# Optimization experiments

Measured on AMD Instinct MI355X. Metric: run time of the kernel, lower is better.

The kernel has to match this reference:

```python
import jax, jax.numpy as jnp
import numpy as np

BN_EPS = 1e-5
LEAKY_SLOPE = 0.01

N_TOTAL, FEAT_DIM = 100000, 128
N_BATCH, K = 50000, 16
EMBED_DIM = 128


def setup_inputs() -> dict:
    key = jax.random.key(0)
    k1, k2, k3 = jax.random.split(key, 3)
    raw_features = jax.random.normal(k1, (N_TOTAL, FEAT_DIM), dtype=jnp.float32)
    weight = jax.random.normal(k2, (FEAT_DIM, EMBED_DIM), dtype=jnp.float32) * (1.0 / np.sqrt(FEAT_DIM))
    gamma = jnp.ones((EMBED_DIM,), dtype=jnp.float32)
    beta = jnp.zeros((EMBED_DIM,), dtype=jnp.float32)
    neigh_idx = jax.random.randint(k3, (N_BATCH, K), 0, N_TOTAL, dtype=jnp.int64)
    return {"raw_features": raw_features, "weight": weight, "gamma": gamma,
            "beta": beta, "neigh_idx": neigh_idx}


def reference(raw_features, weight, gamma, beta, neigh_idx):
    # Mean aggregation over sampled neighbors: [N_BATCH, K, F] -> [N_BATCH, F]
    neigh_feats = jnp.mean(raw_features[neigh_idx], axis=1)
    # Dense transform: [N_BATCH, EMBED_DIM]
    x = neigh_feats @ weight
    # BatchNorm1d (training mode: batch statistics, biased variance)
    mean = jnp.mean(x, axis=0)
    var = jnp.var(x, axis=0)
    x = (x - mean) * jax.lax.rsqrt(var + BN_EPS) * gamma + beta
    # LeakyReLU (default negative_slope=0.01)
    return jnp.where(x >= 0, x, LEAKY_SLOPE * x)
```

## Files before the change

### kernel.cpp

```cpp
#include <hip/hip_runtime.h>
#include <hip/hip_bf16.h>


#define NTOTAL 100000
#define FEAT   128
#define NB     50000
#define KNEI   16
#define NTILES (NB / 16)
#define ZTILES (NTOTAL / 16)
#define NSLOT  8

#define OFF_PSTAT 0
#define OFF_ZB    8192
#define OFF_XB    (8192 + 25600000)
#define WS_NEEDED (OFF_XB + 12800000)

typedef float f32x4 __attribute__((ext_vector_type(4)));
typedef short bf16x8 __attribute__((ext_vector_type(8)));

__device__ __forceinline__ unsigned short f2bf(float f) {
    union { float f; unsigned u; } v; v.f = f;
    unsigned r = v.u + 0x7FFF + ((v.u >> 16) & 1);
    return (unsigned short)(r >> 16);
}

#define WT_LD 136
#define A_LD  136

__global__ __launch_bounds__(256, 4) void enc_zgemm(
    const float* __restrict__ raw, const float* __restrict__ W,
    unsigned short* __restrict__ Zb, float* __restrict__ pstats)
{
    __shared__ unsigned short sWt[128 * WT_LD];
    __shared__ unsigned short sA[16 * A_LD];

    const int t = threadIdx.x;

    if (blockIdx.x == 0) {
        #pragma unroll
        for (int i = 0; i < NSLOT; ++i) pstats[t + i * 256] = 0.f;
    }

    #pragma unroll
    for (int i = 0; i < 16; ++i) {
        int e = t + i * 256;
        float4 w4 = ((const float4*)W)[e];
        int li = e * 4;
        int k = li >> 7, n = li & 127;
        sWt[(n + 0) * WT_LD + k] = f2bf(w4.x);
        sWt[(n + 1) * WT_LD + k] = f2bf(w4.y);
        sWt[(n + 2) * WT_LD + k] = f2bf(w4.z);
        sWt[(n + 3) * WT_LD + k] = f2bf(w4.w);
    }

    const int lane = t & 63;
    const int wv = t >> 6;
    const int ln = lane & 15;
    const int qd = lane >> 4;
    const int c2 = t & 15;
    const int g  = t >> 4;
    const int n0 = wv * 32 + ln, n1 = n0 + 16;

    for (int tile = blockIdx.x; tile < ZTILES; tile += gridDim.x) {
        const int r0 = tile * 16;
        __syncthreads();
        {
            const float4* rp = (const float4*)&raw[(size_t)(r0 + g) * FEAT + c2 * 8];
            float4 x0 = rp[0], x1 = rp[1];
            uint4 b;
            b.x = (unsigned)f2bf(x0.x) | ((unsigned)f2bf(x0.y) << 16);
            b.y = (unsigned)f2bf(x0.z) | ((unsigned)f2bf(x0.w) << 16);
            b.z = (unsigned)f2bf(x1.x) | ((unsigned)f2bf(x1.y) << 16);
            b.w = (unsigned)f2bf(x1.z) | ((unsigned)f2bf(x1.w) << 16);
            *(uint4*)&sA[g * A_LD + c2 * 8] = b;
        }
        __syncthreads();

        f32x4 acc0 = {0.f, 0.f, 0.f, 0.f}, acc1 = {0.f, 0.f, 0.f, 0.f};
        #pragma unroll
        for (int kt = 0; kt < 4; ++kt) {
            const int k0 = kt * 32 + qd * 8;
            bf16x8 a  = *(const bf16x8*)&sA[ln * A_LD + k0];
            bf16x8 b0 = *(const bf16x8*)&sWt[n0 * WT_LD + k0];
            bf16x8 b1 = *(const bf16x8*)&sWt[n1 * WT_LD + k0];
            acc0 = __builtin_amdgcn_mfma_f32_16x16x32_bf16(a, b0, acc0, 0, 0, 0);
            acc1 = __builtin_amdgcn_mfma_f32_16x16x32_bf16(a, b1, acc1, 0, 0, 0);
        }

        #pragma unroll
        for (int ri = 0; ri < 4; ++ri) {
            const int row = r0 + qd * 4 + ri;
            Zb[row * FEAT + n0] = f2bf(acc0[ri]);
            Zb[row * FEAT + n1] = f2bf(acc1[ri]);
        }
    }
}

__global__ __launch_bounds__(256, 4) void enc_gather(
    const unsigned short* __restrict__ Zb, const int* __restrict__ idx,
    unsigned short* __restrict__ xb, float* __restrict__ pstats)
{
    __shared__ int sidx[256];
    __shared__ float sRed[4 * 256];

    const int t = threadIdx.x;
    const int i0 = blockIdx.x * 16;

    sidx[t] = idx[i0 * KNEI + t];
    __syncthreads();

    const int g = t >> 4, c2 = t & 15;
    const int* ip = &sidx[g * KNEI];

    uint4 v[16];
    #pragma unroll
    for (int k = 0; k < KNEI; ++k)
        v[k] = *(const uint4*)&Zb[(size_t)ip[k] * FEAT + c2 * 8];
    __builtin_amdgcn_sched_group_barrier(0x20, 16, 0);
    __builtin_amdgcn_sched_barrier(0);

    float a[8];
    #pragma unroll
    for (int j = 0; j < 8; ++j) a[j] = 0.f;
    #pragma unroll
    for (int k = 0; k < KNEI; ++k) {
        a[0] += __uint_as_float(v[k].x << 16);
        a[1] += __uint_as_float(v[k].x & 0xFFFF0000u);
        a[2] += __uint_as_float(v[k].y << 16);
        a[3] += __uint_as_float(v[k].y & 0xFFFF0000u);
        a[4] += __uint_as_float(v[k].z << 16);
        a[5] += __uint_as_float(v[k].z & 0xFFFF0000u);
        a[6] += __uint_as_float(v[k].w << 16);
        a[7] += __uint_as_float(v[k].w & 0xFFFF0000u);
    }
    #pragma unroll
    for (int j = 0; j < 8; ++j) a[j] *= 0.0625f;

    {
        uint4 b;
        b.x = (unsigned)f2bf(a[0]) | ((unsigned)f2bf(a[1]) << 16);
        b.y = (unsigned)f2bf(a[2]) | ((unsigned)f2bf(a[3]) << 16);
        b.z = (unsigned)f2bf(a[4]) | ((unsigned)f2bf(a[5]) << 16);
        b.w = (unsigned)f2bf(a[6]) | ((unsigned)f2bf(a[7]) << 16);
        *(uint4*)&xb[(size_t)(i0 + g) * FEAT + c2 * 8] = b;
    }

    float q[8];
    #pragma unroll
    for (int j = 0; j < 8; ++j) q[j] = a[j] * a[j];
    #pragma unroll
    for (int j = 0; j < 8; ++j) {
        a[j] += __shfl_down(a[j], 32); a[j] += __shfl_down(a[j], 16);
        q[j] += __shfl_down(q[j], 32); q[j] += __shfl_down(q[j], 16);
    }
    const int lane = t & 63, wv = t >> 6;
    if (lane < 16) {
        #pragma unroll
        for (int j = 0; j < 8; ++j) {
            sRed[wv * 256 + c2 * 8 + j]       = a[j];
            sRed[wv * 256 + 128 + c2 * 8 + j] = q[j];
        }
    }
    __syncthreads();
    float s = sRed[t] + sRed[256 + t] + sRed[512 + t] + sRed[768 + t];
    atomicAdd(&pstats[(blockIdx.x & (NSLOT - 1)) * 256 + t], s);
}

__global__ __launch_bounds__(256) void enc_bn(
    const unsigned short* __restrict__ xb, float* __restrict__ out,
    const float* __restrict__ pstats,
    const float* __restrict__ gamma, const float* __restrict__ beta)
{
    __shared__ float sScale[FEAT], sShift[FEAT];
    const int t = threadIdx.x;
    if (t < FEAT) {
        float s1 = 0.f, s2 = 0.f;
        #pragma unroll
        for (int sl = 0; sl < NSLOT; ++sl) {
            s1 += pstats[sl * 256 + t];
            s2 += pstats[sl * 256 + 128 + t];
        }
        float mean = s1 * (1.0f / NB);
        float var = s2 * (1.0f / NB) - mean * mean;
        float sc = gamma[t] * rsqrtf(var + 1e-5f);
        sScale[t] = sc;
        sShift[t] = beta[t] - mean * sc;
    }
    __syncthreads();

    const int f8 = (t & 15) * 8;
    const float4 sc0 = *(const float4*)&sScale[f8], sc1 = *(const float4*)&sScale[f8 + 4];
    const float4 sh0 = *(const float4*)&sShift[f8], sh1 = *(const float4*)&sShift[f8 + 4];

    const uint4* x4 = (const uint4*)xb;
    float4* o4 = (float4*)out;
    const int total8 = NB * FEAT / 8;
    for (int e = blockIdx.x * 256 + t; e < total8; e += gridDim.x * 256) {
        uint4 v = x4[e];
        float4 r0, r1; float y;
        y = __uint_as_float(v.x << 16)        * sc0.x + sh0.x; r0.x = (y >= 0.f) ? y : 0.01f * y;
        y = __uint_as_float(v.x & 0xFFFF0000u)* sc0.y + sh0.y; r0.y = (y >= 0.f) ? y : 0.01f * y;
        y = __uint_as_float(v.y << 16)        * sc0.z + sh0.z; r0.z = (y >= 0.f) ? y : 0.01f * y;
        y = __uint_as_float(v.y & 0xFFFF0000u)* sc0.w + sh0.w; r0.w = (y >= 0.f) ? y : 0.01f * y;
        y = __uint_as_float(v.z << 16)        * sc1.x + sh1.x; r1.x = (y >= 0.f) ? y : 0.01f * y;
        y = __uint_as_float(v.z & 0xFFFF0000u)* sc1.y + sh1.y; r1.y = (y >= 0.f) ? y : 0.01f * y;
        y = __uint_as_float(v.w << 16)        * sc1.z + sh1.z; r1.z = (y >= 0.f) ? y : 0.01f * y;
        y = __uint_as_float(v.w & 0xFFFF0000u)* sc1.w + sh1.w; r1.w = (y >= 0.f) ? y : 0.01f * y;
        o4[e * 2] = r0; o4[e * 2 + 1] = r1;
    }
}

__global__ __launch_bounds__(256, 4) void enc_gemm_f(
    const float* __restrict__ raw, const float* __restrict__ W,
    const int* __restrict__ idx, float* __restrict__ out,
    float* __restrict__ gstats)
{
    __shared__ unsigned short sWt[128 * WT_LD];
    __shared__ unsigned short sA[16 * A_LD];
    __shared__ int sidx[256];
    const int t = threadIdx.x;
    #pragma unroll 4
    for (int i = 0; i < 64; ++i) {
        int e = t + i * 256;
        int f = e >> 7, n = e & 127;
        sWt[n * WT_LD + f] = f2bf(W[e]);
    }
    const int lane = t & 63, wv = t >> 6, ln = lane & 15, qd = lane >> 4;
    const int c = t & 31, g = t >> 5;
    const int n0 = wv * 32 + ln, n1 = n0 + 16;
    float s1a = 0.f, s2a = 0.f, s1b = 0.f, s2b = 0.f;
    const float4* raw4 = (const float4*)raw;
    for (int tile = blockIdx.x; tile < NTILES; tile += gridDim.x) {
        const int i0 = tile * 16;
        __syncthreads();
        sidx[t] = idx[i0 * KNEI + t];
        __syncthreads();
        #pragma unroll
        for (int rr = 0; rr < 2; ++rr) {
            const int r = g * 2 + rr;
            const int* ip = &sidx[r * KNEI];
            float4 acc = {0.f, 0.f, 0.f, 0.f};
            #pragma unroll
            for (int k = 0; k < KNEI; ++k) {
                float4 v = raw4[(size_t)ip[k] * 32 + c];
                acc.x += v.x; acc.y += v.y; acc.z += v.z; acc.w += v.w;
            }
            ushort4 b;
            b.x = f2bf(acc.x * 0.0625f); b.y = f2bf(acc.y * 0.0625f);
            b.z = f2bf(acc.z * 0.0625f); b.w = f2bf(acc.w * 0.0625f);
            *(ushort4*)&sA[r * A_LD + c * 4] = b;
        }
        __syncthreads();
        f32x4 acc0 = {0.f, 0.f, 0.f, 0.f}, acc1 = {0.f, 0.f, 0.f, 0.f};
        #pragma unroll
        for (int kt = 0; kt < 4; ++kt) {
            const int k0 = kt * 32 + qd * 8;
            bf16x8 a  = *(const bf16x8*)&sA[ln * A_LD + k0];
            bf16x8 b0 = *(const bf16x8*)&sWt[n0 * WT_LD + k0];
            bf16x8 b1 = *(const bf16x8*)&sWt[n1 * WT_LD + k0];
            acc0 = __builtin_amdgcn_mfma_f32_16x16x32_bf16(a, b0, acc0, 0, 0, 0);
            acc1 = __builtin_amdgcn_mfma_f32_16x16x32_bf16(a, b1, acc1, 0, 0, 0);
        }
        #pragma unroll
        for (int ri = 0; ri < 4; ++ri) {
            const int row = i0 + qd * 4 + ri;
            float v0 = acc0[ri], v1 = acc1[ri];
            out[row * FEAT + n0] = v0;
            out[row * FEAT + n1] = v1;
            s1a += v0; s2a += v0 * v0;
            s1b += v1; s2b += v1 * v1;
        }
    }
    s1a += __shfl_down(s1a, 32); s1a += __shfl_down(s1a, 16);
    s2a += __shfl_down(s2a, 32); s2a += __shfl_down(s2a, 16);
    s1b += __shfl_down(s1b, 32); s1b += __shfl_down(s1b, 16);
    s2b += __shfl_down(s2b, 32); s2b += __shfl_down(s2b, 16);
    if (qd == 0) {
        atomicAdd(&gstats[n0], s1a);
        atomicAdd(&gstats[FEAT + n0], s2a);
        atomicAdd(&gstats[n1], s1b);
        atomicAdd(&gstats[FEAT + n1], s2b);
    }
}

__global__ __launch_bounds__(256) void enc_bn_f(
    float* __restrict__ out, const float* __restrict__ gstats,
    const float* __restrict__ gamma, const float* __restrict__ beta)
{
    __shared__ float sScale[FEAT], sShift[FEAT];
    const int t = threadIdx.x;
    if (t < FEAT) {
        float s1 = gstats[t], s2 = gstats[FEAT + t];
        float mean = s1 * (1.0f / NB);
        float var = s2 * (1.0f / NB) - mean * mean;
        float sc = gamma[t] * rsqrtf(var + 1e-5f);
        sScale[t] = sc;
        sShift[t] = beta[t] - mean * sc;
    }
    __syncthreads();
    const int f4 = (t & 31) * 4;
    const float4 sc = *(const float4*)&sScale[f4];
    const float4 sh = *(const float4*)&sShift[f4];
    const int total4 = NB * FEAT / 4;
    float4* o4 = (float4*)out;
    for (int e = blockIdx.x * 256 + t; e < total4; e += gridDim.x * 256) {
        float4 v = o4[e];
        float4 r; float y;
        y = v.x * sc.x + sh.x; r.x = (y >= 0.f) ? y : 0.01f * y;
        y = v.y * sc.y + sh.y; r.y = (y >= 0.f) ? y : 0.01f * y;
        y = v.z * sc.z + sh.z; r.z = (y >= 0.f) ? y : 0.01f * y;
        y = v.w * sc.w + sh.w; r.w = (y >= 0.f) ? y : 0.01f * y;
        o4[e] = r;
    }
}

extern "C" void kernel_launch(void* const* d_in, const int* in_sizes, int n_in,
                              void* d_out, int out_size, void* d_ws, size_t ws_size,
                              hipStream_t stream) {
    const float* raw   = (const float*)d_in[0];
    const float* W     = (const float*)d_in[1];
    const float* gamma = (const float*)d_in[2];
    const float* beta  = (const float*)d_in[3];
    const int*   idx   = (const int*)d_in[4];
    float* out = (float*)d_out;

    char* ws = (char*)d_ws;

    if (ws_size >= WS_NEEDED) {
        float* pstats        = (float*)(ws + OFF_PSTAT);
        unsigned short* Zb   = (unsigned short*)(ws + OFF_ZB);
        unsigned short* xb   = (unsigned short*)(ws + OFF_XB);
        enc_zgemm<<<1042, 256, 0, stream>>>(raw, W, Zb, pstats);
        enc_gather<<<NTILES, 256, 0, stream>>>(Zb, idx, xb, pstats);
        enc_bn<<<1024, 256, 0, stream>>>(xb, out, pstats, gamma, beta);
    } else {
        float* gstats = (float*)(ws + OFF_PSTAT);
        hipMemsetAsync(gstats, 0, 2 * FEAT * sizeof(float), stream);
        enc_gemm_f<<<1024, 256, 0, stream>>>(raw, W, idx, out, gstats);
        enc_bn_f<<<1024, 256, 0, stream>>>(out, gstats, gamma, beta);
    }
}
```

Measured before the change: 152.3 us.

## Fuse GEMM, gather and batchnorm into one cooperative kernel with grid syncs

```diff
diff --git a/kernel.cpp b/kernel.cpp
--- a/kernel.cpp
+++ b/kernel.cpp
@@ -1,5 +1,8 @@
 #include <hip/hip_runtime.h>
 #include <hip/hip_bf16.h>
+#include <hip/hip_cooperative_groups.h>
+
+namespace cg = cooperative_groups;
 
 
 #define NTOTAL 100000
@@ -9,6 +12,7 @@
 #define NTILES (NB / 16)
 #define ZTILES (NTOTAL / 16)
 #define NSLOT  8
+#define TMAX   4
 
 #define OFF_PSTAT 0
 #define OFF_ZB    8192
@@ -26,14 +30,22 @@
 
 #define WT_LD 136
 #define A_LD  136
-
-__global__ __launch_bounds__(256, 4) void enc_zgemm(
+#define SMEM_BYTES 39168
+
+__global__ __launch_bounds__(256, 4) void enc_all(
     const float* __restrict__ raw, const float* __restrict__ W,
+    const float* __restrict__ gamma, const float* __restrict__ beta,
+    const int* __restrict__ idx, float* __restrict__ out,
     unsigned short* __restrict__ Zb, float* __restrict__ pstats)
 {
-    __shared__ unsigned short sWt[128 * WT_LD];
-    __shared__ unsigned short sA[16 * A_LD];
-
+    __shared__ __align__(16) char smem[SMEM_BYTES];
+    unsigned short* sWt = (unsigned short*)smem;
+    unsigned short* sA  = (unsigned short*)(smem + 34816);
+    int*   sidx = (int*)smem;
+    float* sRed = (float*)(smem + 1024);
+    float* sSS  = (float*)smem;
+
+    cg::grid_group grid = cg::this_grid();
     const int t = threadIdx.x;
 
     if (blockIdx.x == 0) {
@@ -94,6 +106,176 @@
             Zb[row * FEAT + n1] = f2bf(acc1[ri]);
         }
     }
+    grid.sync();
+
+    uint4 xr0 = {0,0,0,0}, xr1 = {0,0,0,0}, xr2 = {0,0,0,0}, xr3 = {0,0,0,0};
+    float s1[8], s2[8];
+    #pragma unroll
+    for (int j = 0; j < 8; ++j) { s1[j] = 0.f; s2[j] = 0.f; }
+
+    #pragma unroll
+    for (int tt = 0; tt < TMAX; ++tt) {
+        const int tile = blockIdx.x + tt * gridDim.x;
+        if (tile < NTILES) {
+            __syncthreads();
+            sidx[t] = idx[tile * 16 * KNEI + t];
+            __syncthreads();
+
+            const int* ip = &sidx[g * KNEI];
+            uint4 v[16];
+            #pragma unroll
+            for (int k = 0; k < KNEI; ++k)
+                v[k] = *(const uint4*)&Zb[(size_t)ip[k] * FEAT + c2 * 8];
+            __builtin_amdgcn_sched_barrier(0);
+
+            float a[8];
+            #pragma unroll
+            for (int j = 0; j < 8; ++j) a[j] = 0.f;
+            #pragma unroll
+            for (int k = 0; k < KNEI; ++k) {
+                a[0] += __uint_as_float(v[k].x << 16);
+                a[1] += __uint_as_float(v[k].x & 0xFFFF0000u);
+                a[2] += __uint_as_float(v[k].y << 16);
+                a[3] += __uint_as_float(v[k].y & 0xFFFF0000u);
+                a[4] += __uint_as_float(v[k].z << 16);
+                a[5] += __uint_as_float(v[k].z & 0xFFFF0000u);
+                a[6] += __uint_as_float(v[k].w << 16);
+                a[7] += __uint_as_float(v[k].w & 0xFFFF0000u);
+            }
+            #pragma unroll
+            for (int j = 0; j < 8; ++j) a[j] *= 0.0625f;
+
+            #pragma unroll
+            for (int j = 0; j < 8; ++j) { s1[j] += a[j]; s2[j] += a[j] * a[j]; }
+
+            uint4 b;
+            b.x = (unsigned)f2bf(a[0]) | ((unsigned)f2bf(a[1]) << 16);
+            b.y = (unsigned)f2bf(a[2]) | ((unsigned)f2bf(a[3]) << 16);
+            b.z = (unsigned)f2bf(a[4]) | ((unsigned)f2bf(a[5]) << 16);
+            b.w = (unsigned)f2bf(a[6]) | ((unsigned)f2bf(a[7]) << 16);
+            if (tt == 0) xr0 = b;
+            else if (tt == 1) xr1 = b;
+            else if (tt == 2) xr2 = b;
+            else xr3 = b;
+        }
+    }
+
+    #pragma unroll
+    for (int j = 0; j < 8; ++j) {
+        s1[j] += __shfl_down(s1[j], 32); s1[j] += __shfl_down(s1[j], 16);
+        s2[j] += __shfl_down(s2[j], 32); s2[j] += __shfl_down(s2[j], 16);
+    }
+    __syncthreads();
+    if (lane < 16) {
+        #pragma unroll
+        for (int j = 0; j < 8; ++j) {
+            sRed[wv * 256 + c2 * 8 + j]       = s1[j];
+            sRed[wv * 256 + 128 + c2 * 8 + j] = s2[j];
+        }
+    }
+    __syncthreads();
+    {
+        float s = sRed[t] + sRed[256 + t] + sRed[512 + t] + sRed[768 + t];
+        atomicAdd(&pstats[(blockIdx.x & (NSLOT - 1)) * 256 + t], s);
+    }
+    grid.sync();
+
+    if (t < FEAT) {
+        float a1 = 0.f, a2 = 0.f;
+        #pragma unroll
+        for (int sl = 0; sl < NSLOT; ++sl) {
+            a1 += pstats[sl * 256 + t];
+            a2 += pstats[sl * 256 + 128 + t];
+        }
+        float mean = a1 * (1.0f / NB);
+        float var = a2 * (1.0f / NB) - mean * mean;
+        float sc = gamma[t] * rsqrtf(var + 1e-5f);
+        sSS[t] = sc;
+        sSS[FEAT + t] = beta[t] - mean * sc;
+    }
+    __syncthreads();
+
+    const int f8 = c2 * 8;
+    const float4 sc0 = *(const float4*)&sSS[f8], sc1 = *(const float4*)&sSS[f8 + 4];
+    const float4 sh0 = *(const float4*)&sSS[FEAT + f8], sh1 = *(const float4*)&sSS[FEAT + f8 + 4];
+
+    #pragma unroll
+    for (int tt = 0; tt < TMAX; ++tt) {
+        const int tile = blockIdx.x + tt * gridDim.x;
+        if (tile < NTILES) {
+            uint4 v = (tt == 0) ? xr0 : (tt == 1) ? xr1 : (tt == 2) ? xr2 : xr3;
+            float4 r0, r1; float y;
+            y = __uint_as_float(v.x << 16)        * sc0.x + sh0.x; r0.x = (y >= 0.f) ? y : 0.01f * y;
+            y = __uint_as_float(v.x & 0xFFFF0000u)* sc0.y + sh0.y; r0.y = (y >= 0.f) ? y : 0.01f * y;
+            y = __uint_as_float(v.y << 16)        * sc0.z + sh0.z; r0.z = (y >= 0.f) ? y : 0.01f * y;
+            y = __uint_as_float(v.y & 0xFFFF0000u)* sc0.w + sh0.w; r0.w = (y >= 0.f) ? y : 0.01f * y;
+            y = __uint_as_float(v.z << 16)        * sc1.x + sh1.x; r1.x = (y >= 0.f) ? y : 0.01f * y;
+            y = __uint_as_float(v.z & 0xFFFF0000u)* sc1.y + sh1.y; r1.y = (y >= 0.f) ? y : 0.01f * y;
+            y = __uint_as_float(v.w << 16)        * sc1.z + sh1.z; r1.z = (y >= 0.f) ? y : 0.01f * y;
+            y = __uint_as_float(v.w & 0xFFFF0000u)* sc1.w + sh1.w; r1.w = (y >= 0.f) ? y : 0.01f * y;
+            float4* op = (float4*)&out[(size_t)(tile * 16 + g) * FEAT + f8];
+            op[0] = r0; op[1] = r1;
+        }
+    }
+}
+
+__global__ __launch_bounds__(256, 4) void enc_zgemm(
+    const float* __restrict__ raw, const float* __restrict__ W,
+    unsigned short* __restrict__ Zb, float* __restrict__ pstats)
+{
+    __shared__ unsigned short sWt[128 * WT_LD];
+    __shared__ unsigned short sA[16 * A_LD];
+    const int t = threadIdx.x;
+    if (blockIdx.x == 0) {
+        #pragma unroll
+        for (int i = 0; i < NSLOT; ++i) pstats[t + i * 256] = 0.f;
+    }
+    #pragma unroll
+    for (int i = 0; i < 16; ++i) {
+        int e = t + i * 256;
+        float4 w4 = ((const float4*)W)[e];
+        int li = e * 4;
+        int k = li >> 7, n = li & 127;
+        sWt[(n + 0) * WT_LD + k] = f2bf(w4.x);
+        sWt[(n + 1) * WT_LD + k] = f2bf(w4.y);
+        sWt[(n + 2) * WT_LD + k] = f2bf(w4.z);
+        sWt[(n + 3) * WT_LD + k] = f2bf(w4.w);
+    }
+    const int lane = t & 63;
+    const int wv = t >> 6, ln = lane & 15, qd = lane >> 4;
+    const int c2 = t & 15, g = t >> 4;
+    const int n0 = wv * 32 + ln, n1 = n0 + 16;
+    for (int tile = blockIdx.x; tile < ZTILES; tile += gridDim.x) {
+        const int r0 = tile * 16;
+        __syncthreads();
+        {
+            const float4* rp = (const float4*)&raw[(size_t)(r0 + g) * FEAT + c2 * 8];
+            float4 x0 = rp[0], x1 = rp[1];
+            uint4 b;
+            b.x = (unsigned)f2bf(x0.x) | ((unsigned)f2bf(x0.y) << 16);
+            b.y = (unsigned)f2bf(x0.z) | ((unsigned)f2bf(x0.w) << 16);
+            b.z = (unsigned)f2bf(x1.x) | ((unsigned)f2bf(x1.y) << 16);
+            b.w = (unsigned)f2bf(x1.z) | ((unsigned)f2bf(x1.w) << 16);
+            *(uint4*)&sA[g * A_LD + c2 * 8] = b;
+        }
+        __syncthreads();
+        f32x4 acc0 = {0.f, 0.f, 0.f, 0.f}, acc1 = {0.f, 0.f, 0.f, 0.f};
+        #pragma unroll
+        for (int kt = 0; kt < 4; ++kt) {
+            const int k0 = kt * 32 + qd * 8;
+            bf16x8 a  = *(const bf16x8*)&sA[ln * A_LD + k0];
+            bf16x8 b0 = *(const bf16x8*)&sWt[n0 * WT_LD + k0];
+            bf16x8 b1 = *(const bf16x8*)&sWt[n1 * WT_LD + k0];
+            acc0 = __builtin_amdgcn_mfma_f32_16x16x32_bf16(a, b0, acc0, 0, 0, 0);
+            acc1 = __builtin_amdgcn_mfma_f32_16x16x32_bf16(a, b1, acc1, 0, 0, 0);
+        }
+        #pragma unroll
+        for (int ri = 0; ri < 4; ++ri) {
+            const int row = r0 + qd * 4 + ri;
+            Zb[row * FEAT + n0] = f2bf(acc0[ri]);
+            Zb[row * FEAT + n1] = f2bf(acc1[ri]);
+        }
+    }
 }
 
 __global__ __launch_bounds__(256, 4) void enc_gather(
@@ -102,23 +284,17 @@
 {
     __shared__ int sidx[256];
     __shared__ float sRed[4 * 256];
-
     const int t = threadIdx.x;
     const int i0 = blockIdx.x * 16;
-
     sidx[t] = idx[i0 * KNEI + t];
     __syncthreads();
-
     const int g = t >> 4, c2 = t & 15;
     const int* ip = &sidx[g * KNEI];
-
     uint4 v[16];
     #pragma unroll
     for (int k = 0; k < KNEI; ++k)
         v[k] = *(const uint4*)&Zb[(size_t)ip[k] * FEAT + c2 * 8];
-    __builtin_amdgcn_sched_group_barrier(0x20, 16, 0);
     __builtin_amdgcn_sched_barrier(0);
-
     float a[8];
     #pragma unroll
     for (int j = 0; j < 8; ++j) a[j] = 0.f;
@@ -135,7 +311,6 @@
     }
     #pragma unroll
     for (int j = 0; j < 8; ++j) a[j] *= 0.0625f;
-
     {
         uint4 b;
         b.x = (unsigned)f2bf(a[0]) | ((unsigned)f2bf(a[1]) << 16);
@@ -144,7 +319,6 @@
         b.w = (unsigned)f2bf(a[6]) | ((unsigned)f2bf(a[7]) << 16);
         *(uint4*)&xb[(size_t)(i0 + g) * FEAT + c2 * 8] = b;
     }
-
     float q[8];
     #pragma unroll
     for (int j = 0; j < 8; ++j) q[j] = a[j] * a[j];
@@ -187,11 +361,9 @@
         sShift[t] = beta[t] - mean * sc;
     }
     __syncthreads();
-
     const int f8 = (t & 15) * 8;
     const float4 sc0 = *(const float4*)&sScale[f8], sc1 = *(const float4*)&sScale[f8 + 4];
     const float4 sh0 = *(const float4*)&sShift[f8], sh1 = *(const float4*)&sShift[f8 + 4];
-
     const uint4* x4 = (const uint4*)xb;
     float4* o4 = (float4*)out;
     const int total8 = NB * FEAT / 8;
@@ -325,11 +497,36 @@
     float* out = (float*)d_out;
 
     char* ws = (char*)d_ws;
+    float* pstats      = (float*)(ws + OFF_PSTAT);
+    unsigned short* Zb = (unsigned short*)(ws + OFF_ZB);
+    unsigned short* xb = (unsigned short*)(ws + OFF_XB);
+
+    static int coopGrid = -1;
+    if (coopGrid < 0) {
+        int g = 0, dev = 0, occ = 0;
+        hipDeviceProp_t prop;
+        if (hipGetDevice(&dev) == hipSuccess &&
+            hipGetDeviceProperties(&prop, dev) == hipSuccess &&
+            prop.cooperativeLaunch &&
+            hipOccupancyMaxActiveBlocksPerMultiprocessor(&occ, enc_all, 256, 0) == hipSuccess &&
+            occ > 0) {
+            g = occ * prop.multiProcessorCount;
+            if (g > 1024) g = 1024;
+        }
+        if (g * TMAX < NTILES) g = 0;
+        coopGrid = g;
+    }
+
+    if (ws_size >= WS_NEEDED && coopGrid > 0) {
+        void* args[] = { (void*)&raw, (void*)&W, (void*)&gamma, (void*)&beta,
+                         (void*)&idx, (void*)&out, (void*)&Zb, (void*)&pstats };
+        hipError_t e = hipLaunchCooperativeKernel(enc_all, dim3(coopGrid), dim3(256),
+                                                  args, 0u, stream);
+        if (e == hipSuccess) return;
+        coopGrid = 0;
+    }
 
     if (ws_size >= WS_NEEDED) {
-        float* pstats        = (float*)(ws + OFF_PSTAT);
-        unsigned short* Zb   = (unsigned short*)(ws + OFF_ZB);
-        unsigned short* xb   = (unsigned short*)(ws + OFF_XB);
         enc_zgemm<<<1042, 256, 0, stream>>>(raw, W, Zb, pstats);
         enc_gather<<<NTILES, 256, 0, stream>>>(Zb, idx, xb, pstats);
         enc_bn<<<1024, 256, 0, stream>>>(xb, out, pstats, gamma, beta);
```

New measurement: 152.0 us. No clear change (-0.2%).

## Store projected features in column slabs and gather per 16-feature slab

Applied to the files above, without the earlier changes.

```diff
diff --git a/kernel.cpp b/kernel.cpp
--- a/kernel.cpp
+++ b/kernel.cpp
@@ -9,14 +9,16 @@
 #define NTILES (NB / 16)
 #define ZTILES (NTOTAL / 16)
 #define NSLOT  8
+#define NSTRIPE ((NB + 127) / 128)
 
 #define OFF_PSTAT 0
-#define OFF_ZB    8192
+#define OFF_ZC    8192
 #define OFF_XB    (8192 + 25600000)
 #define WS_NEEDED (OFF_XB + 12800000)
 
 typedef float f32x4 __attribute__((ext_vector_type(4)));
 typedef short bf16x8 __attribute__((ext_vector_type(8)));
+typedef int   i32x4 __attribute__((ext_vector_type(4)));
 
 __device__ __forceinline__ unsigned short f2bf(float f) {
     union { float f; unsigned u; } v; v.f = f;
@@ -26,10 +28,11 @@
 
 #define WT_LD 136
 #define A_LD  136
+#define SLAB_ELEMS ((size_t)NTOTAL * 16)
 
 __global__ __launch_bounds__(256, 4) void enc_zgemm(
     const float* __restrict__ raw, const float* __restrict__ W,
-    unsigned short* __restrict__ Zb, float* __restrict__ pstats)
+    unsigned short* __restrict__ Zc, float* __restrict__ pstats)
 {
     __shared__ unsigned short sWt[128 * WT_LD];
     __shared__ unsigned short sA[16 * A_LD];
@@ -60,6 +63,7 @@
     const int c2 = t & 15;
     const int g  = t >> 4;
     const int n0 = wv * 32 + ln, n1 = n0 + 16;
+    const int s0 = wv * 2, s1 = wv * 2 + 1;
 
     for (int tile = blockIdx.x; tile < ZTILES; tile += gridDim.x) {
         const int r0 = tile * 16;
@@ -90,59 +94,74 @@
         #pragma unroll
         for (int ri = 0; ri < 4; ++ri) {
             const int row = r0 + qd * 4 + ri;
-            Zb[row * FEAT + n0] = f2bf(acc0[ri]);
-            Zb[row * FEAT + n1] = f2bf(acc1[ri]);
-        }
-    }
-}
-
-__global__ __launch_bounds__(256, 4) void enc_gather(
-    const unsigned short* __restrict__ Zb, const int* __restrict__ idx,
+            Zc[(size_t)s0 * SLAB_ELEMS + (size_t)row * 16 + ln] = f2bf(acc0[ri]);
+            Zc[(size_t)s1 * SLAB_ELEMS + (size_t)row * 16 + ln] = f2bf(acc1[ri]);
+        }
+    }
+}
+
+__global__ __launch_bounds__(256, 4) void enc_gather_slab(
+    const unsigned short* __restrict__ Zc, const int* __restrict__ idx,
     unsigned short* __restrict__ xb, float* __restrict__ pstats)
 {
-    __shared__ int sidx[256];
-    __shared__ float sRed[4 * 256];
-
-    const int t = threadIdx.x;
-    const int i0 = blockIdx.x * 16;
-
-    sidx[t] = idx[i0 * KNEI + t];
+    __shared__ int sidx[2048];
+    __shared__ float sRed[128];
+
+    const int t = threadIdx.x;
+    const int fc = blockIdx.x & 7;
+    const int stripe = blockIdx.x >> 3;
+    const int r0 = stripe * 128;
+
+    {
+        const int base = r0 * KNEI + t * 8;
+        if (base + 7 < NB * KNEI) {
+            const i32x4* g4 = (const i32x4*)&idx[base];
+            i32x4 v0 = __builtin_nontemporal_load(&g4[0]);
+            i32x4 v1 = __builtin_nontemporal_load(&g4[1]);
+            *(i32x4*)&sidx[t * 8]     = v0;
+            *(i32x4*)&sidx[t * 8 + 4] = v1;
+        }
+    }
     __syncthreads();
 
-    const int g = t >> 4, c2 = t & 15;
-    const int* ip = &sidx[g * KNEI];
-
-    uint4 v[16];
-    #pragma unroll
-    for (int k = 0; k < KNEI; ++k)
-        v[k] = *(const uint4*)&Zb[(size_t)ip[k] * FEAT + c2 * 8];
-    __builtin_amdgcn_sched_group_barrier(0x20, 16, 0);
-    __builtin_amdgcn_sched_barrier(0);
+    const int r = t >> 1;
+    const int h = t & 1;
+    const int row = r0 + r;
+    const bool valid = row < NB;
+
+    const unsigned short* slab = Zc + (size_t)fc * SLAB_ELEMS;
 
     float a[8];
     #pragma unroll
     for (int j = 0; j < 8; ++j) a[j] = 0.f;
-    #pragma unroll
-    for (int k = 0; k < KNEI; ++k) {
-        a[0] += __uint_as_float(v[k].x << 16);
-        a[1] += __uint_as_float(v[k].x & 0xFFFF0000u);
-        a[2] += __uint_as_float(v[k].y << 16);
-        a[3] += __uint_as_float(v[k].y & 0xFFFF0000u);
-        a[4] += __uint_as_float(v[k].z << 16);
-        a[5] += __uint_as_float(v[k].z & 0xFFFF0000u);
-        a[6] += __uint_as_float(v[k].w << 16);
-        a[7] += __uint_as_float(v[k].w & 0xFFFF0000u);
-    }
-    #pragma unroll
-    for (int j = 0; j < 8; ++j) a[j] *= 0.0625f;
-
-    {
+
+    if (valid) {
+        const int* ip = &sidx[r * KNEI];
+        uint4 v[16];
+        #pragma unroll
+        for (int k = 0; k < KNEI; ++k)
+            v[k] = *(const uint4*)&slab[(size_t)ip[k] * 16 + h * 8];
+        __builtin_amdgcn_sched_barrier(0);
+        #pragma unroll
+        for (int k = 0; k < KNEI; ++k) {
+            a[0] += __uint_as_float(v[k].x << 16);
+            a[1] += __uint_as_float(v[k].x & 0xFFFF0000u);
+            a[2] += __uint_as_float(v[k].y << 16);
+            a[3] += __uint_as_float(v[k].y & 0xFFFF0000u);
+            a[4] += __uint_as_float(v[k].z << 16);
+            a[5] += __uint_as_float(v[k].z & 0xFFFF0000u);
+            a[6] += __uint_as_float(v[k].w << 16);
+            a[7] += __uint_as_float(v[k].w & 0xFFFF0000u);
+        }
+        #pragma unroll
+        for (int j = 0; j < 8; ++j) a[j] *= 0.0625f;
+
         uint4 b;
         b.x = (unsigned)f2bf(a[0]) | ((unsigned)f2bf(a[1]) << 16);
         b.y = (unsigned)f2bf(a[2]) | ((unsigned)f2bf(a[3]) << 16);
         b.z = (unsigned)f2bf(a[4]) | ((unsigned)f2bf(a[5]) << 16);
         b.w = (unsigned)f2bf(a[6]) | ((unsigned)f2bf(a[7]) << 16);
-        *(uint4*)&xb[(size_t)(i0 + g) * FEAT + c2 * 8] = b;
+        *(uint4*)&xb[(size_t)row * FEAT + fc * 16 + h * 8] = b;
     }
 
     float q[8];
@@ -150,20 +169,28 @@
     for (int j = 0; j < 8; ++j) q[j] = a[j] * a[j];
     #pragma unroll
     for (int j = 0; j < 8; ++j) {
-        a[j] += __shfl_down(a[j], 32); a[j] += __shfl_down(a[j], 16);
-        q[j] += __shfl_down(q[j], 32); q[j] += __shfl_down(q[j], 16);
+        a[j] += __shfl_down(a[j], 32); q[j] += __shfl_down(q[j], 32);
+        a[j] += __shfl_down(a[j], 16); q[j] += __shfl_down(q[j], 16);
+        a[j] += __shfl_down(a[j], 8);  q[j] += __shfl_down(q[j], 8);
+        a[j] += __shfl_down(a[j], 4);  q[j] += __shfl_down(q[j], 4);
+        a[j] += __shfl_down(a[j], 2);  q[j] += __shfl_down(q[j], 2);
     }
     const int lane = t & 63, wv = t >> 6;
-    if (lane < 16) {
+    if (lane < 2) {
         #pragma unroll
         for (int j = 0; j < 8; ++j) {
-            sRed[wv * 256 + c2 * 8 + j]       = a[j];
-            sRed[wv * 256 + 128 + c2 * 8 + j] = q[j];
+            sRed[wv * 16 + h * 8 + j]      = a[j];
+            sRed[64 + wv * 16 + h * 8 + j] = q[j];
         }
     }
     __syncthreads();
-    float s = sRed[t] + sRed[256 + t] + sRed[512 + t] + sRed[768 + t];
-    atomicAdd(&pstats[(blockIdx.x & (NSLOT - 1)) * 256 + t], s);
+    if (t < 16) {
+        float u1 = sRed[t] + sRed[16 + t] + sRed[32 + t] + sRed[48 + t];
+        float u2 = sRed[64 + t] + sRed[80 + t] + sRed[96 + t] + sRed[112 + t];
+        const int slot = stripe & (NSLOT - 1);
+        atomicAdd(&pstats[slot * 256 + fc * 16 + t], u1);
+        atomicAdd(&pstats[slot * 256 + 128 + fc * 16 + t], u2);
+    }
 }
 
 __global__ __launch_bounds__(256) void enc_bn(
@@ -327,15 +354,15 @@
     char* ws = (char*)d_ws;
 
     if (ws_size >= WS_NEEDED) {
-        float* pstats        = (float*)(ws + OFF_PSTAT);
-        unsigned short* Zb   = (unsigned short*)(ws + OFF_ZB);
-        unsigned short* xb   = (unsigned short*)(ws + OFF_XB);
-        enc_zgemm<<<1042, 256, 0, stream>>>(raw, W, Zb, pstats);
-        enc_gather<<<NTILES, 256, 0, stream>>>(Zb, idx, xb, pstats);
+        float* pstats      = (float*)(ws + OFF_PSTAT);
+        unsigned short* Zc = (unsigned short*)(ws + OFF_ZC);
+        unsigned short* xb = (unsigned short*)(ws + OFF_XB);
+        enc_zgemm<<<1042, 256, 0, stream>>>(raw, W, Zc, pstats);
+        enc_gather_slab<<<NSTRIPE * 8, 256, 0, stream>>>(Zc, idx, xb, pstats);
         enc_bn<<<1024, 256, 0, stream>>>(xb, out, pstats, gamma, beta);
     } else {
         float* gstats = (float*)(ws + OFF_PSTAT);
-        hipMemsetAsync(gstats, 0, 2 * FEAT * sizeof(float), stream);
+        (void)hipMemsetAsync(gstats, 0, 2 * FEAT * sizeof(float), stream);
         enc_gemm_f<<<1024, 256, 0, stream>>>(raw, W, idx, out, gstats);
         enc_bn_f<<<1024, 256, 0, stream>>>(out, gstats, gamma, beta);
     }
```

Result: slower. 164.7 us (+8.2%).
